# Kernel optimization log

Hardware: AMD Instinct MI355X
Metric: run time of the kernel (lower is better)

## Reference

```python
import jax, jax.numpy as jnp
import numpy as np

HID = 10
IN_DIM = 256
B, H, W = 8, 96, 96


def _conv(x, w, b=None, pad=0):
    y = jax.lax.conv_general_dilated(x, w, (1, 1), [(pad, pad), (pad, pad)],
                                     dimension_numbers=('NCHW', 'OIHW', 'NCHW'))
    return y if b is None else y + b[None, :, None, None]


def _bn(x, g, b):
    # eval-mode InPlaceABN(Sync) with identity running stats -> per-channel affine
    return x * g[None, :, None, None] + b[None, :, None, None]


def _branch(x, w1, g1, b1, w2, g2, b2):
    # Conv3x3 -> BN -> ReLU -> Conv1x1 -> BN -> ReLU  (relation / comp_u / comp_l)
    y = jax.nn.relu(_bn(_conv(x, w1, pad=1), g1, b1))
    return jax.nn.relu(_bn(_conv(y, w2), g2, b2))


def _gru(x, h, gw, gb, cw, cg, cb):
    # ConvGRU with 1x1 kernels
    gates = _conv(jnp.concatenate([x, h], axis=1), gw, gb)
    r = jax.nn.sigmoid(gates[:, 0:1])
    u = jax.nn.sigmoid(gates[:, 1:2])
    cnm = jax.nn.relu(_bn(_conv(jnp.concatenate([x, r * h], axis=1), cw), cg, cb))
    return (1.0 - u) * h + u * cnm


def setup_inputs():
    key = jax.random.key(0)
    ks = iter(jax.random.split(key, 48))

    def nrm(shape, s=0.05):
        return jax.random.normal(next(ks), shape, jnp.float32) * s

    inp = {
        'f_nodes': jax.random.normal(next(ks), (2, B, HID, H, W), jnp.float32),
        'h_nodes': jax.random.normal(next(ks), (3, B, HID, H, W), jnp.float32),
        'p_nodes': jax.random.normal(next(ks), (7, B, HID, H, W), jnp.float32),
        'xh': jax.random.normal(next(ks), (B, IN_DIM, H, W), jnp.float32),
        'f_atts': jax.random.uniform(next(ks), (2, B, 1, H, W), jnp.float32),
        'p_atts': jax.random.uniform(next(ks), (7, B, 1, H, W), jnp.float32),
        # Decomposition.decomp_att: Conv3x3(257->256)+BN+ReLU, Conv1x1(256->2)+bias
        'da_w1': nrm((IN_DIM, IN_DIM + 1, 3, 3)),
        'da_g1': jnp.ones((IN_DIM,), jnp.float32),
        'da_b1': jnp.zeros((IN_DIM,), jnp.float32),
        'da_w2': nrm((2, IN_DIM, 1, 1)),
        'da_b2': jnp.zeros((2,), jnp.float32),
    }
    # relation (shared across children), comp_u, comp_l: Conv3x3(20->10)+BN+ReLU, Conv1x1(10->10)+BN+ReLU
    for p in ('rel', 'cu', 'cl'):
        inp[p + '_w1'] = nrm((HID, 2 * HID, 3, 3))
        inp[p + '_g1'] = jnp.ones((HID,), jnp.float32)
        inp[p + '_b1'] = jnp.zeros((HID,), jnp.float32)
        inp[p + '_w2'] = nrm((HID, HID, 1, 1))
        inp[p + '_g2'] = jnp.ones((HID,), jnp.float32)
        inp[p + '_b2'] = jnp.zeros((HID,), jnp.float32)
    # 3 ConvGRUs (cls_h), 1x1 kernels, stacked on leading dim
    inp['gru_gw'] = nrm((3, 2, 2 * HID, 1, 1))
    inp['gru_gb'] = jnp.zeros((3, 2), jnp.float32)
    inp['gru_cw'] = nrm((3, HID, 2 * HID, 1, 1))
    inp['gru_cg'] = jnp.ones((3, HID), jnp.float32)
    inp['gru_cb'] = jnp.zeros((3, HID), jnp.float32)
    return inp


def reference(f_nodes, h_nodes, p_nodes, xh, f_atts, p_atts,
              da_w1, da_g1, da_b1, da_w2, da_b2,
              rel_w1, rel_g1, rel_b1, rel_w2, rel_g2, rel_b2,
              cu_w1, cu_g1, cu_b1, cu_w2, cu_g2, cu_b2,
              cl_w1, cl_g1, cl_b1, cl_w2, cl_g2, cl_b2,
              gru_gw, gru_gb, gru_cw, gru_cg, gru_cb):
    parent, parent_att = f_nodes[1], f_atts[1]
    # Decomposition of full-body node into 2 half nodes
    dm = _conv(jnp.concatenate([parent_att, xh], axis=1), da_w1, pad=1)
    dm = jax.nn.relu(_bn(dm, da_g1, da_b1))
    dm = _conv(dm, da_w2, da_b2)  # [B, 2, H, W] decomposition map
    datt = jax.nn.softmax(dm, axis=1)
    decomp = [_branch(jnp.concatenate([parent * datt[:, i:i + 1] * parent_att,
                                       h_nodes[1 + i]], axis=1),
                      rel_w1, rel_g1, rel_b1, rel_w2, rel_g2, rel_b2)
              for i in range(2)]
    # node 0: background
    n0 = _gru(f_nodes[0] + p_nodes[0], h_nodes[0],
              gru_gw[0], gru_gb[0], gru_cw[0], gru_cg[0], gru_cb[0])
    # node 1: upper half = composition(upper parts 1-4) + decomposition
    up = jnp.sum(p_nodes[1:5], axis=0) * jnp.sum(p_atts[1:5], axis=0)
    comp_u = _branch(jnp.concatenate([h_nodes[1], up], axis=1),
                     cu_w1, cu_g1, cu_b1, cu_w2, cu_g2, cu_b2)
    n1 = _gru(comp_u + decomp[0], h_nodes[1],
              gru_gw[1], gru_gb[1], gru_cw[1], gru_cg[1], gru_cb[1])
    # node 2: lower half = composition(lower parts 5-6) + decomposition
    lo = jnp.sum(p_nodes[5:7], axis=0) * jnp.sum(p_atts[5:7], axis=0)
    comp_l = _branch(jnp.concatenate([h_nodes[2], lo], axis=1),
                     cl_w1, cl_g1, cl_b1, cl_w2, cl_g2, cl_b2)
    n2 = _gru(comp_l + decomp[1], h_nodes[2],
              gru_gw[2], gru_gb[2], gru_cw[2], gru_cg[2], gru_cb[2])
    return (jnp.stack([n0, n1, n2]), dm)
```

## Files before the change

### kernel.cpp

```cpp
#include <hip/hip_runtime.h>
#include <cstddef>
#include <cstdint>

constexpr int Bn    = 8;
constexpr int Hn    = 96;
constexpr int Wn    = 96;
constexpr int HWn   = Hn * Wn;
constexpr int BHWn  = Bn * HWn;
constexpr int B10HW = Bn * 10 * HWn;

using short8  = __attribute__((ext_vector_type(8))) short;
using ushort8 = __attribute__((ext_vector_type(8))) unsigned short;
using float4v = __attribute__((ext_vector_type(4))) float;

__device__ __forceinline__ unsigned short f2bf(float f) {
    unsigned u = __builtin_bit_cast(unsigned, f);
    u += 0x7FFFu + ((u >> 16) & 1u);
    return (unsigned short)(u >> 16);
}

__global__ void k_packw(const float* __restrict__ w1, short* __restrict__ wpk)
{
    const int idx = blockIdx.x * 256 + threadIdx.x;
    if (idx >= 592128) return;
    const int co  = idx / 2313;
    const int rem = idx % 2313;
    const int ci  = rem / 9;
    const int tap = rem % 9;
    const int cb  = ci >> 5;
    const int g   = (ci >> 3) & 3;
    const int j   = ci & 7;
    const int q   = co >> 4;
    const int lane = (co & 15) + (g << 4);
    const int t   = cb * 9 + tap;
    wpk[(((size_t)t * 16 + q) * 64 + lane) * 8 + j] = (short)f2bf(w1[idx]);
}

__global__ __launch_bounds__(256, 3)
void k_bigconv3(const float* __restrict__ xh, const float* __restrict__ patt,
                const short* __restrict__ wpk, const float* __restrict__ g1,
                const float* __restrict__ b1, const float* __restrict__ w2,
                const float* __restrict__ db2,
                float* __restrict__ dm_out, float* __restrict__ s01)
{
    __shared__ __align__(16) short xs[2][4][137][8];
    __shared__ float part[4][64][2];

    const int tid  = threadIdx.x;
    const int lane = tid & 63;
    const int wid  = tid >> 6;
    const int bx   = blockIdx.x;
    const int wseg = bx % 3;
    const int hb   = (bx / 3) % 48;
    const int b    = bx / 144;
    const int h0   = hb * 2, w0 = wseg * 32;
    const int am   = lane & 15;
    const int aq   = lane >> 4;

    float4v acc[4][4];
    #pragma unroll
    for (int i = 0; i < 4; ++i)
        #pragma unroll
        for (int j = 0; j < 4; ++j)
            acc[i][j] = float4v{0.f, 0.f, 0.f, 0.f};

    int arow[4], acol[4];
    #pragma unroll
    for (int mt = 0; mt < 4; ++mt) {
        const int m = mt * 16 + am;
        arow[mt] = m >> 5;
        acol[mt] = m & 31;
    }

    auto stageX = [&](int cb, int buf) {
        const int cig0 = cb * 32 + wid * 8;
        for (int pos = lane; pos < 136; pos += 64) {
            const int row = pos / 34, col = pos % 34;
            const int hh = h0 - 1 + row, ww = w0 - 1 + col;
            const bool inb = ((unsigned)hh < (unsigned)Hn) & ((unsigned)ww < (unsigned)Wn);
            const int off = hh * Wn + ww;
            ushort8 v;
            #pragma unroll
            for (int j = 0; j < 8; ++j) {
                const int ci = cig0 + j;
                float f = 0.f;
                if (inb && ci < 257)
                    f = (ci == 0) ? patt[b * HWn + off]
                                  : xh[((size_t)b * 256 + (ci - 1)) * HWn + off];
                v[j] = f2bf(f);
            }
            *(ushort8*)&xs[buf][wid][pos][0] = v;
        }
    };

    const short8* wp = (const short8*)wpk;
    const int qb = wid * 4;

    stageX(0, 0);
    short8 bfr[4], bnx[4];
    #pragma unroll
    for (int nt = 0; nt < 4; ++nt)
        bfr[nt] = wp[(size_t)(qb + nt) * 64 + lane];
    __syncthreads();

    for (int cb = 0; cb < 9; ++cb) {
        const int buf = cb & 1;
        for (int tap = 0; tap < 9; ++tap) {
            const int t = cb * 9 + tap;
            if (t < 80) {
                #pragma unroll
                for (int nt = 0; nt < 4; ++nt)
                    bnx[nt] = wp[((size_t)(t + 1) * 16 + qb + nt) * 64 + lane];
            }
            const int kh = tap / 3, kw = tap % 3;
            short8 afr[4];
            #pragma unroll
            for (int mt = 0; mt < 4; ++mt) {
                const int pos = (arow[mt] + kh) * 34 + (acol[mt] + kw);
                afr[mt] = *(const short8*)&xs[buf][aq][pos][0];
            }
            #pragma unroll
            for (int mt = 0; mt < 4; ++mt)
                #pragma unroll
                for (int nt = 0; nt < 4; ++nt)
                    acc[mt][nt] = __builtin_amdgcn_mfma_f32_16x16x32_bf16(
                        afr[mt], bfr[nt], acc[mt][nt], 0, 0, 0);
            #pragma unroll
            for (int nt = 0; nt < 4; ++nt) bfr[nt] = bnx[nt];
        }
        if (cb < 8) stageX(cb + 1, buf ^ 1);
        __syncthreads();
    }

    float gv[4], bv[4], wa[4], wbv[4];
    #pragma unroll
    for (int nt = 0; nt < 4; ++nt) {
        const int co = wid * 64 + nt * 16 + am;
        gv[nt]  = g1[co];
        bv[nt]  = b1[co];
        wa[nt]  = w2[co];
        wbv[nt] = w2[256 + co];
    }
    #pragma unroll
    for (int mt = 0; mt < 4; ++mt) {
        #pragma unroll
        for (int reg = 0; reg < 4; ++reg) {
            float s0 = 0.f, s1 = 0.f;
            #pragma unroll
            for (int nt = 0; nt < 4; ++nt) {
                const float y = fmaxf(fmaf(acc[mt][nt][reg], gv[nt], bv[nt]), 0.f);
                s0 = fmaf(wa[nt], y, s0);
                s1 = fmaf(wbv[nt], y, s1);
            }
            #pragma unroll
            for (int off = 1; off < 16; off <<= 1) {
                s0 += __shfl_xor(s0, off, 64);
                s1 += __shfl_xor(s1, off, 64);
            }
            if (am == 0) {
                const int m = mt * 16 + aq * 4 + reg;
                part[wid][m][0] = s0;
                part[wid][m][1] = s1;
            }
        }
    }
    __syncthreads();
    if (tid < 64) {
        const int m = tid, r = m >> 5, c = m & 31;
        const int off = (h0 + r) * Wn + (w0 + c);
        float d0 = part[0][m][0] + part[1][m][0] + part[2][m][0] + part[3][m][0] + db2[0];
        float d1 = part[0][m][1] + part[1][m][1] + part[2][m][1] + part[3][m][1] + db2[1];
        dm_out[(size_t)(b * 2) * HWn + off]     = d0;
        dm_out[(size_t)(b * 2 + 1) * HWn + off] = d1;
        const float mx = fmaxf(d0, d1);
        const float e0 = expf(d0 - mx), e1 = expf(d1 - mx);
        const float pa = patt[b * HWn + off];
        const float inv = pa / (e0 + e1);
        s01[b * HWn + off]        = e0 * inv;
        s01[BHWn + b * HWn + off] = e1 * inv;
    }
}

__global__ void k_uplo(const float* __restrict__ pn, const float* __restrict__ pa,
                       float* __restrict__ up, float* __restrict__ lo)
{
    const int c = blockIdx.y;
    const int i = blockIdx.x * 256 + threadIdx.x;
    if (i >= BHWn / 4) return;
    const int b = i / (HWn / 4), q = i % (HWn / 4);
    const float4v* PA = (const float4v*)pa;
    const float4v* PN = (const float4v*)pn;
    float4v au = {0, 0, 0, 0}, al = {0, 0, 0, 0};
    #pragma unroll
    for (int k = 1; k <= 4; ++k) au += PA[(size_t)(k * Bn + b) * (HWn / 4) + q];
    #pragma unroll
    for (int k = 5; k <= 6; ++k) al += PA[(size_t)(k * Bn + b) * (HWn / 4) + q];
    float4v su = {0, 0, 0, 0}, sl = {0, 0, 0, 0};
    #pragma unroll
    for (int k = 1; k <= 4; ++k) su += PN[((size_t)(k * Bn + b) * 10 + c) * (HWn / 4) + q];
    #pragma unroll
    for (int k = 5; k <= 6; ++k) sl += PN[((size_t)(k * Bn + b) * 10 + c) * (HWn / 4) + q];
    ((float4v*)up)[((size_t)b * 10 + c) * (HWn / 4) + q] = su * au;
    ((float4v*)lo)[((size_t)b * 10 + c) * (HWn / 4) + q] = sl * al;
}

struct BranchW  { const float *w1, *g1, *b1, *w2, *g2, *b2; };
struct BranchW3 { BranchW p[3]; };

__global__ __launch_bounds__(256)
void k_branch(BranchW3 P, const float* __restrict__ parent, const float* __restrict__ h_nodes,
              const float* __restrict__ s01, const float* __restrict__ up,
              const float* __restrict__ lo, float* __restrict__ bout)
{
    const int z  = blockIdx.y;
    const int pi = (z < 2) ? 0 : (z - 1);
    __shared__ float xt[20][10][34];
    __shared__ __align__(16) float wlt[9 * 20 * 12];
    __shared__ float w2l[100], g1l[10], b1l[10], g2l[10], b2l[10];

    const BranchW& Pw = P.p[pi];
    const int tid = threadIdx.x;
    for (int idx = tid; idx < 2160; idx += 256) {
        const int co = idx % 12, rem = idx / 12, ci = rem % 20, tap = rem / 20;
        wlt[idx] = (co < 10) ? Pw.w1[(co * 20 + ci) * 9 + tap] : 0.f;
    }
    if (tid < 100) w2l[tid] = Pw.w2[tid];
    if (tid < 10) {
        g1l[tid] = Pw.g1[tid]; b1l[tid] = Pw.b1[tid];
        g2l[tid] = Pw.g2[tid]; b2l[tid] = Pw.b2[tid];
    }

    const int bx = blockIdx.x;
    const int tw = bx % 3, th = (bx / 3) % 12, b = bx / 36;
    const int h0 = th * 8, w0 = tw * 32;

    const float* Ab;
    const float* sc = nullptr;
    const float* Bb;
    if (z == 0)      { Ab = parent; sc = s01;        Bb = h_nodes + (size_t)1 * B10HW; }
    else if (z == 1) { Ab = parent; sc = s01 + BHWn; Bb = h_nodes + (size_t)2 * B10HW; }
    else if (z == 2) { Ab = h_nodes + (size_t)1 * B10HW; Bb = up; }
    else             { Ab = h_nodes + (size_t)2 * B10HW; Bb = lo; }

    for (int idx = tid; idx < 6800; idx += 256) {
        const int col = idx % 34, rem = idx / 34, row = rem % 10, ch = rem / 10;
        const int hh = h0 - 1 + row, ww = w0 - 1 + col;
        float v = 0.f;
        if (((unsigned)hh < (unsigned)Hn) & ((unsigned)ww < (unsigned)Wn)) {
            const int off = hh * Wn + ww;
            if (ch < 10) {
                v = Ab[((size_t)b * 10 + ch) * HWn + off];
                if (sc) v *= sc[b * HWn + off];
            } else {
                v = Bb[((size_t)b * 10 + (ch - 10)) * HWn + off];
            }
        }
        ((float*)xt)[idx] = v;
    }
    __syncthreads();

    const int r = tid >> 5, c = tid & 31;
    float a0 = 0, a1 = 0, a2 = 0, a3 = 0, a4 = 0, a5 = 0, a6 = 0, a7 = 0, a8 = 0, a9 = 0;
    #pragma unroll
    for (int tap = 0; tap < 9; ++tap) {
        const int kh = tap / 3, kw = tap % 3;
        #pragma unroll
        for (int ci = 0; ci < 20; ++ci) {
            const float xv = xt[ci][r + kh][c + kw];
            const float4 wA = *(const float4*)&wlt[(tap * 20 + ci) * 12];
            const float4 wB = *(const float4*)&wlt[(tap * 20 + ci) * 12 + 4];
            const float2 wC = *(const float2*)&wlt[(tap * 20 + ci) * 12 + 8];
            a0 = fmaf(wA.x, xv, a0); a1 = fmaf(wA.y, xv, a1);
            a2 = fmaf(wA.z, xv, a2); a3 = fmaf(wA.w, xv, a3);
            a4 = fmaf(wB.x, xv, a4); a5 = fmaf(wB.y, xv, a5);
            a6 = fmaf(wB.z, xv, a6); a7 = fmaf(wB.w, xv, a7);
            a8 = fmaf(wC.x, xv, a8); a9 = fmaf(wC.y, xv, a9);
        }
    }
    float acc[10] = {a0, a1, a2, a3, a4, a5, a6, a7, a8, a9};
    float y[10];
    #pragma unroll
    for (int co = 0; co < 10; ++co)
        y[co] = fmaxf(fmaf(acc[co], g1l[co], b1l[co]), 0.f);
    const int hw = (h0 + r) * Wn + (w0 + c);
    #pragma unroll
    for (int co = 0; co < 10; ++co) {
        float s = 0.f;
        #pragma unroll
        for (int i = 0; i < 10; ++i) s = fmaf(w2l[co * 10 + i], y[i], s);
        s = fmaxf(fmaf(s, g2l[co], b2l[co]), 0.f);
        bout[(size_t)z * B10HW + ((size_t)b * 10 + co) * HWn + hw] = s;
    }
}

__global__ void k_gru(const float* __restrict__ f_nodes, const float* __restrict__ h_nodes,
                      const float* __restrict__ p_nodes, const float* __restrict__ bout,
                      const float* __restrict__ gw, const float* __restrict__ gb,
                      const float* __restrict__ cw, const float* __restrict__ cg,
                      const float* __restrict__ cb, float* __restrict__ out)
{
    const int z = blockIdx.y;
    __shared__ float gwl[40], cwl[200], gbl[2], cgl[10], cbl[10];
    if (threadIdx.x < 40)  gwl[threadIdx.x] = gw[z * 40 + threadIdx.x];
    if (threadIdx.x < 200) cwl[threadIdx.x] = cw[z * 200 + threadIdx.x];
    if (threadIdx.x < 2)   gbl[threadIdx.x] = gb[z * 2 + threadIdx.x];
    if (threadIdx.x < 10) {
        cgl[threadIdx.x] = cg[z * 10 + threadIdx.x];
        cbl[threadIdx.x] = cb[z * 10 + threadIdx.x];
    }
    __syncthreads();

    const int p = blockIdx.x * 256 + threadIdx.x;
    const int b = p / HWn, hw = p % HWn;
    float x[10], h[10];
    #pragma unroll
    for (int c = 0; c < 10; ++c) {
        const size_t idx = ((size_t)b * 10 + c) * HWn + hw;
        if (z == 0)      x[c] = f_nodes[idx] + p_nodes[idx];
        else if (z == 1) x[c] = bout[(size_t)2 * B10HW + idx] + bout[idx];
        else             x[c] = bout[(size_t)3 * B10HW + idx] + bout[(size_t)1 * B10HW + idx];
        h[c] = h_nodes[(size_t)z * B10HW + idx];
    }
    float g0 = gbl[0], g1 = gbl[1];
    #pragma unroll
    for (int c = 0; c < 10; ++c) {
        g0 = fmaf(gwl[c],      x[c], g0);
        g0 = fmaf(gwl[10 + c], h[c], g0);
        g1 = fmaf(gwl[20 + c], x[c], g1);
        g1 = fmaf(gwl[30 + c], h[c], g1);
    }
    const float r = 1.f / (1.f + expf(-g0));
    const float u = 1.f / (1.f + expf(-g1));
    #pragma unroll
    for (int o = 0; o < 10; ++o) {
        float s = 0.f;
        #pragma unroll
        for (int c = 0; c < 10; ++c) {
            s = fmaf(cwl[o * 20 + c],      x[c],     s);
            s = fmaf(cwl[o * 20 + 10 + c], r * h[c], s);
        }
        s = fmaxf(fmaf(s, cgl[o], cbl[o]), 0.f);
        out[(size_t)z * B10HW + ((size_t)b * 10 + o) * HWn + hw] =
            (1.f - u) * h[o] + u * s;
    }
}

extern "C" void kernel_launch(void* const* d_in, const int* in_sizes, int n_in,
                              void* d_out, int out_size, void* d_ws, size_t ws_size,
                              hipStream_t stream)
{
    (void)in_sizes; (void)n_in; (void)out_size; (void)ws_size;

    const float* f_nodes = (const float*)d_in[0];
    const float* h_nodes = (const float*)d_in[1];
    const float* p_nodes = (const float*)d_in[2];
    const float* xh      = (const float*)d_in[3];
    const float* f_atts  = (const float*)d_in[4];
    const float* p_atts  = (const float*)d_in[5];
    const float* da_w1   = (const float*)d_in[6];
    const float* da_g1   = (const float*)d_in[7];
    const float* da_b1   = (const float*)d_in[8];
    const float* da_w2   = (const float*)d_in[9];
    const float* da_b2   = (const float*)d_in[10];

    BranchW3 P;
    for (int i = 0; i < 3; ++i) {
        P.p[i].w1 = (const float*)d_in[11 + 6 * i + 0];
        P.p[i].g1 = (const float*)d_in[11 + 6 * i + 1];
        P.p[i].b1 = (const float*)d_in[11 + 6 * i + 2];
        P.p[i].w2 = (const float*)d_in[11 + 6 * i + 3];
        P.p[i].g2 = (const float*)d_in[11 + 6 * i + 4];
        P.p[i].b2 = (const float*)d_in[11 + 6 * i + 5];
    }
    const float* gru_gw = (const float*)d_in[29];
    const float* gru_gb = (const float*)d_in[30];
    const float* gru_cw = (const float*)d_in[31];
    const float* gru_cg = (const float*)d_in[32];
    const float* gru_cb = (const float*)d_in[33];

    float* out    = (float*)d_out;
    float* dm_out = out + (size_t)3 * B10HW;

    float* ws     = (float*)d_ws;
    float* s01    = ws;
    float* up     = s01 + 2 * BHWn;
    float* lo     = up + B10HW;
    float* bout   = lo + B10HW;
    short* wpk    = (short*)bout;

    const float* patt   = f_atts + BHWn;
    const float* parent = f_nodes + B10HW;

    hipMemsetAsync(wpk, 0, (size_t)82944 * 8 * sizeof(short), stream);
    k_packw<<<dim3(2313), 256, 0, stream>>>(da_w1, wpk);
    k_bigconv3<<<dim3(1152), 256, 0, stream>>>(xh, patt, wpk, da_g1, da_b1,
                                               da_w2, da_b2, dm_out, s01);
    k_uplo<<<dim3(72, 10), 256, 0, stream>>>(p_nodes, p_atts, up, lo);
    k_branch<<<dim3(288, 4), 256, 0, stream>>>(P, parent, h_nodes, s01, up, lo, bout);
    k_gru<<<dim3(288, 3), 256, 0, stream>>>(f_nodes, h_nodes, p_nodes, bout,
                                            gru_gw, gru_gb, gru_cg ? gru_cw : gru_cw,
                                            gru_cg, gru_cb, out);
}
```

Before: 390.9 us.

## Fuse up/lo reduction into branch kernel, pack weights gather-style, reorder conv blocks

```diff
diff --git a/kernel.cpp b/kernel.cpp
--- a/kernel.cpp
+++ b/kernel.cpp
@@ -21,19 +21,17 @@
 
 __global__ void k_packw(const float* __restrict__ w1, short* __restrict__ wpk)
 {
-    const int idx = blockIdx.x * 256 + threadIdx.x;
-    if (idx >= 592128) return;
-    const int co  = idx / 2313;
-    const int rem = idx % 2313;
-    const int ci  = rem / 9;
-    const int tap = rem % 9;
-    const int cb  = ci >> 5;
-    const int g   = (ci >> 3) & 3;
-    const int j   = ci & 7;
-    const int q   = co >> 4;
-    const int lane = (co & 15) + (g << 4);
-    const int t   = cb * 9 + tap;
-    wpk[(((size_t)t * 16 + q) * 64 + lane) * 8 + j] = (short)f2bf(w1[idx]);
+    const int o = blockIdx.x * 256 + threadIdx.x;
+    if (o >= 663552) return;
+    const int j    = o & 7;
+    const int lane = (o >> 3) & 63;
+    const int q    = (o >> 9) & 15;
+    const int t    = o >> 13;
+    const int co   = q * 16 + (lane & 15);
+    const int ci   = (t / 9) * 32 + ((lane >> 4) & 3) * 8 + j;
+    const int tap  = t % 9;
+    const float f  = (ci < 257) ? w1[((size_t)co * 257 + ci) * 9 + tap] : 0.f;
+    wpk[o] = (short)f2bf(f);
 }
 
 __global__ __launch_bounds__(256, 3)
@@ -50,9 +48,10 @@
     const int lane = tid & 63;
     const int wid  = tid >> 6;
     const int bx   = blockIdx.x;
-    const int wseg = bx % 3;
-    const int hb   = (bx / 3) % 48;
-    const int b    = bx / 144;
+    const int b    = bx & 7;
+    const int r2   = bx >> 3;
+    const int wseg = r2 % 3;
+    const int hb   = r2 / 3;
     const int h0   = hb * 2, w0 = wseg * 32;
     const int am   = lane & 15;
     const int aq   = lane >> 4;
@@ -181,40 +180,18 @@
     }
 }
 
-__global__ void k_uplo(const float* __restrict__ pn, const float* __restrict__ pa,
-                       float* __restrict__ up, float* __restrict__ lo)
-{
-    const int c = blockIdx.y;
-    const int i = blockIdx.x * 256 + threadIdx.x;
-    if (i >= BHWn / 4) return;
-    const int b = i / (HWn / 4), q = i % (HWn / 4);
-    const float4v* PA = (const float4v*)pa;
-    const float4v* PN = (const float4v*)pn;
-    float4v au = {0, 0, 0, 0}, al = {0, 0, 0, 0};
-    #pragma unroll
-    for (int k = 1; k <= 4; ++k) au += PA[(size_t)(k * Bn + b) * (HWn / 4) + q];
-    #pragma unroll
-    for (int k = 5; k <= 6; ++k) al += PA[(size_t)(k * Bn + b) * (HWn / 4) + q];
-    float4v su = {0, 0, 0, 0}, sl = {0, 0, 0, 0};
-    #pragma unroll
-    for (int k = 1; k <= 4; ++k) su += PN[((size_t)(k * Bn + b) * 10 + c) * (HWn / 4) + q];
-    #pragma unroll
-    for (int k = 5; k <= 6; ++k) sl += PN[((size_t)(k * Bn + b) * 10 + c) * (HWn / 4) + q];
-    ((float4v*)up)[((size_t)b * 10 + c) * (HWn / 4) + q] = su * au;
-    ((float4v*)lo)[((size_t)b * 10 + c) * (HWn / 4) + q] = sl * al;
-}
-
 struct BranchW  { const float *w1, *g1, *b1, *w2, *g2, *b2; };
 struct BranchW3 { BranchW p[3]; };
 
 __global__ __launch_bounds__(256)
 void k_branch(BranchW3 P, const float* __restrict__ parent, const float* __restrict__ h_nodes,
-              const float* __restrict__ s01, const float* __restrict__ up,
-              const float* __restrict__ lo, float* __restrict__ bout)
+              const float* __restrict__ s01, const float* __restrict__ pn,
+              const float* __restrict__ pa, float* __restrict__ bout)
 {
     const int z  = blockIdx.y;
     const int pi = (z < 2) ? 0 : (z - 1);
     __shared__ float xt[20][10][34];
+    __shared__ float paSum[340];
     __shared__ __align__(16) float wlt[9 * 20 * 12];
     __shared__ float w2l[100], g1l[10], b1l[10], g2l[10], b2l[10];
 
@@ -236,11 +213,27 @@
 
     const float* Ab;
     const float* sc = nullptr;
-    const float* Bb;
+    const float* Bb = nullptr;
+    int k0 = 0, k1 = -1;
     if (z == 0)      { Ab = parent; sc = s01;        Bb = h_nodes + (size_t)1 * B10HW; }
     else if (z == 1) { Ab = parent; sc = s01 + BHWn; Bb = h_nodes + (size_t)2 * B10HW; }
-    else if (z == 2) { Ab = h_nodes + (size_t)1 * B10HW; Bb = up; }
-    else             { Ab = h_nodes + (size_t)2 * B10HW; Bb = lo; }
+    else if (z == 2) { Ab = h_nodes + (size_t)1 * B10HW; k0 = 1; k1 = 4; }
+    else             { Ab = h_nodes + (size_t)2 * B10HW; k0 = 5; k1 = 6; }
+
+    if (z >= 2) {
+        for (int idx = tid; idx < 340; idx += 256) {
+            const int col = idx % 34, row = idx / 34;
+            const int hh = h0 - 1 + row, ww = w0 - 1 + col;
+            float s = 0.f;
+            if (((unsigned)hh < (unsigned)Hn) & ((unsigned)ww < (unsigned)Wn)) {
+                const int off = hh * Wn + ww;
+                for (int k = k0; k <= k1; ++k)
+                    s += pa[(size_t)(k * Bn + b) * HWn + off];
+            }
+            paSum[idx] = s;
+        }
+    }
+    __syncthreads();
 
     for (int idx = tid; idx < 6800; idx += 256) {
         const int col = idx % 34, rem = idx / 34, row = rem % 10, ch = rem / 10;
@@ -251,8 +244,13 @@
             if (ch < 10) {
                 v = Ab[((size_t)b * 10 + ch) * HWn + off];
                 if (sc) v *= sc[b * HWn + off];
+            } else if (z < 2) {
+                v = Bb[((size_t)b * 10 + (ch - 10)) * HWn + off];
             } else {
-                v = Bb[((size_t)b * 10 + (ch - 10)) * HWn + off];
+                float s = 0.f;
+                for (int k = k0; k <= k1; ++k)
+                    s += pn[((size_t)(k * Bn + b) * 10 + (ch - 10)) * HWn + off];
+                v = s * paSum[row * 34 + col];
             }
         }
         ((float*)xt)[idx] = v;
@@ -383,21 +381,17 @@
 
     float* ws     = (float*)d_ws;
     float* s01    = ws;
-    float* up     = s01 + 2 * BHWn;
-    float* lo     = up + B10HW;
-    float* bout   = lo + B10HW;
+    float* bout   = s01 + 2 * BHWn;
     short* wpk    = (short*)bout;
 
     const float* patt   = f_atts + BHWn;
     const float* parent = f_nodes + B10HW;
 
-    hipMemsetAsync(wpk, 0, (size_t)82944 * 8 * sizeof(short), stream);
-    k_packw<<<dim3(2313), 256, 0, stream>>>(da_w1, wpk);
+    k_packw<<<dim3(2592), 256, 0, stream>>>(da_w1, wpk);
     k_bigconv3<<<dim3(1152), 256, 0, stream>>>(xh, patt, wpk, da_g1, da_b1,
                                                da_w2, da_b2, dm_out, s01);
-    k_uplo<<<dim3(72, 10), 256, 0, stream>>>(p_nodes, p_atts, up, lo);
-    k_branch<<<dim3(288, 4), 256, 0, stream>>>(P, parent, h_nodes, s01, up, lo, bout);
+    k_branch<<<dim3(288, 4), 256, 0, stream>>>(P, parent, h_nodes, s01,
+                                               p_nodes, p_atts, bout);
     k_gru<<<dim3(288, 3), 256, 0, stream>>>(f_nodes, h_nodes, p_nodes, bout,
-                                            gru_gw, gru_gb, gru_cg ? gru_cw : gru_cw,
-                                            gru_cg, gru_cb, out);
-}
+                                            gru_gw, gru_gb, gru_cw, gru_cg, gru_cb, out);
+}
```

Result: no change. 387.4 us (-0.9%).
